# Optimization experiments

Hardware: AMD Instinct MI355X
Metric: run time of the kernel (lower is better)

## Reference

```python
import jax, jax.numpy as jnp
import numpy as np

B, N = 128, 128                      # graphs, nodes per graph (complete graphs)
D_IN, H, D_MP = 6, 32, 64            # GCN dims
SLOPE = 0.1                          # leaky_relu negative slope
E_UD = N * (N - 1) // 2              # undirected edges per graph
SMAT_IDX = np.array([0, 1, 2, 3, 1, 4, 5, 6, 2, 5, 7, 8, 3, 6, 8, 9])  # 10-vec -> sym 4x4


def setup_inputs():
    key = jax.random.key(0)
    ks = jax.random.split(key, 20)
    total = B * N
    # complete-graph connectivity (same topology for every graph, offset per graph)
    iu0, iu1 = np.triu_indices(N, 1)
    s = np.concatenate([iu0, iu1])
    d = np.concatenate([iu1, iu0])
    off = (np.arange(B) * N)[:, None]
    edge_index = np.stack([(off + s[None, :]).ravel(), (off + d[None, :]).ravel()])
    em = np.zeros((N, N), np.int32)
    em[iu0, iu1] = np.arange(E_UD)
    em[iu1, iu0] = np.arange(E_UD)
    ud_edges = np.stack([iu0, iu1], axis=1)

    def p(k, shape):
        return jax.random.normal(k, shape, jnp.float32) * 0.1

    return {
        "x": jax.random.normal(ks[0], (total, D_IN), jnp.float32),
        "edge_index": jnp.asarray(edge_index, jnp.int32),
        "edge_map": jnp.asarray(em, jnp.int32),
        "ud_edges": jnp.asarray(ud_edges, jnp.int32),
        # GCN stack 6->32->32->64
        "Wg0": p(ks[1], (D_IN, H)), "bg0": jnp.zeros((H,), jnp.float32),
        "Wg1": p(ks[2], (H, H)),    "bg1": jnp.zeros((H,), jnp.float32),
        "Wg2": p(ks[3], (H, D_MP)), "bg2": jnp.zeros((D_MP,), jnp.float32),
        # node MLP 64->64->64->10
        "Wn0": p(ks[4], (D_MP, D_MP)), "bn0": jnp.zeros((D_MP,), jnp.float32),
        "Wn1": p(ks[5], (D_MP, D_MP)), "bn1": jnp.zeros((D_MP,), jnp.float32),
        "Wn2": p(ks[6], (D_MP, 10)),   "bn2": jnp.zeros((10,), jnp.float32),
        # edge MLP 128->128->128->16
        "We0": p(ks[7], (2 * D_MP, 2 * D_MP)), "be0": jnp.zeros((2 * D_MP,), jnp.float32),
        "We1": p(ks[8], (2 * D_MP, 2 * D_MP)), "be1": jnp.zeros((2 * D_MP,), jnp.float32),
        "We2": p(ks[9], (2 * D_MP, 16)),       "be2": jnp.zeros((16,), jnp.float32),
    }


def _lrelu(h):
    return jnp.where(h >= 0, h, SLOPE * h)


def reference(x, edge_index, edge_map, ud_edges,
              Wg0, bg0, Wg1, bg1, Wg2, bg2,
              Wn0, bn0, Wn1, bn1, Wn2, bn2,
              We0, be0, We1, be1, We2, be2):
    total = x.shape[0]
    src, dst = edge_index[0], edge_index[1]
    x = x[:, :D_IN]  # node_feature_mode == 1

    # symmetric GCN normalization (no self loops): norm_e = deg_src^-1/2 * deg_dst^-1/2
    deg = jax.ops.segment_sum(jnp.ones(src.shape[0], x.dtype), dst, num_segments=total)
    dinv = jax.lax.rsqrt(jnp.maximum(deg, 1e-12))
    norm = (dinv[src] * dinv[dst])[:, None]

    def gcn(h, W, b):
        m = (h @ W)[src] * norm
        return jax.ops.segment_sum(m, dst, num_segments=total) + b

    h = _lrelu(gcn(x, Wg0, bg0))   # dropout skipped (eval mode)
    h = _lrelu(gcn(h, Wg1, bg1))
    h = gcn(h, Wg2, bg2)           # [total, 64]

    xb = h.reshape(B, N, D_MP)

    # batched node MLP (original loops per node)
    v = _lrelu(xb @ Wn0 + bn0)
    v = _lrelu(v @ Wn1 + bn1)
    v = v @ Wn2 + bn2              # [B, N, 10]

    # batched edge MLP for (i,j) ordering (original loops per edge; e_tril is
    # computed but discarded upstream since recover_factor is called with e_triu twice)
    xi = xb[:, ud_edges[:, 0]]
    xj = xb[:, ud_edges[:, 1]]
    e = jnp.concatenate([xi, xj], axis=-1)   # [B, E_UD, 128]
    e = _lrelu(e @ We0 + be0)
    e = _lrelu(e @ We1 + be1)
    e = e @ We2 + be2                        # [B, E_UD, 16]

    # assemble U: off-diagonal 4x4 blocks from e (both triangles), diagonal smat(v)
    blocks = e[:, edge_map]                  # [B, N, N, 16]
    diag = v[:, :, SMAT_IDX]                 # [B, N, 16]
    idx = jnp.arange(N)
    blocks = blocks.at[:, idx, idx].set(diag)
    U = blocks.reshape(B, N, N, 4, 4).transpose(0, 1, 3, 2, 4).reshape(B, 4 * N, 4 * N)
    return (h, U)
```

## Files before the change

### kernel.cpp

```cpp
#include <hip/hip_runtime.h>
#include <hip/hip_bf16.h>

#define LRELU(v) ((v) >= 0.f ? (v) : 0.1f*(v))

typedef float  f32x4 __attribute__((ext_vector_type(4)));
typedef short  s16x8 __attribute__((ext_vector_type(8)));
typedef int    i32x4 __attribute__((ext_vector_type(4)));
typedef unsigned short ushort_t;
typedef unsigned int   u32;

constexpr float GNORM = 1.0f/127.0f;

#define MFMA(d, a, b) d = __builtin_amdgcn_mfma_f32_16x16x32_bf16(a, b, d, 0, 0, 0)

__device__ __forceinline__ ushort_t f2bf(float v) {
    return __builtin_bit_cast(ushort_t, __float2bfloat16(v));
}
__device__ __forceinline__ float bf2f(ushort_t u) {
    return __builtin_bit_cast(float, (u32)u << 16);
}

__global__ __launch_bounds__(128) void k_gcn(
    const float* __restrict__ x,
    const float* __restrict__ Wg0, const float* __restrict__ bg0,
    const float* __restrict__ Wg1, const float* __restrict__ bg1,
    const float* __restrict__ Wg2, const float* __restrict__ bg2,
    float* __restrict__ hout)
{
    __shared__ __align__(16) float w0[192], w1[1024], w2[2048];
    __shared__ float bb0[32], bb1[32], bb2[64];
    __shared__ float ta[128][65];
    __shared__ float part[4][64];
    __shared__ float S[64];
    const int v = threadIdx.x;
    const int b = blockIdx.x;

    for (int idx = v; idx < 192;  idx += 128) w0[idx] = Wg0[idx];
    for (int idx = v; idx < 1024; idx += 128) w1[idx] = Wg1[idx];
    for (int idx = v; idx < 2048; idx += 128) w2[idx] = Wg2[idx];
    if (v < 32) { bb0[v] = bg0[v]; bb1[v] = bg1[v]; }
    if (v < 64) bb2[v] = bg2[v];

    float xv[6];
    #pragma unroll
    for (int k = 0; k < 6; ++k) xv[k] = x[(b*128 + v)*6 + k];
    __syncthreads();

    float t0[32];
    #pragma unroll
    for (int n = 0; n < 32; ++n) {
        float a = 0.f;
        #pragma unroll
        for (int k = 0; k < 6; ++k) a += xv[k]*w0[k*32+n];
        t0[n] = a;
        ta[v][n] = a;
    }
    __syncthreads();
    { const int g = v >> 5, d = v & 31;
      float p = 0.f;
      for (int r = 0; r < 32; ++r) p += ta[g*32+r][d];
      part[g][d] = p; }
    __syncthreads();
    if (v < 32) S[v] = part[0][v]+part[1][v]+part[2][v]+part[3][v];
    __syncthreads();
    float h1[32];
    #pragma unroll
    for (int n = 0; n < 32; ++n) {
        float hv = (S[n] - t0[n])*GNORM + bb0[n];
        h1[n] = LRELU(hv);
    }
    __syncthreads();

    float t1[32];
    #pragma unroll
    for (int n = 0; n < 32; ++n) t1[n] = 0.f;
    for (int k = 0; k < 32; ++k) {
        const float hk = h1[k];
        #pragma unroll
        for (int n4 = 0; n4 < 8; ++n4) {
            const float4 w = *(const float4*)&w1[k*32 + n4*4];
            t1[n4*4+0] += hk*w.x; t1[n4*4+1] += hk*w.y;
            t1[n4*4+2] += hk*w.z; t1[n4*4+3] += hk*w.w;
        }
    }
    #pragma unroll
    for (int n = 0; n < 32; ++n) ta[v][n] = t1[n];
    __syncthreads();
    { const int g = v >> 5, d = v & 31;
      float p = 0.f;
      for (int r = 0; r < 32; ++r) p += ta[g*32+r][d];
      part[g][d] = p; }
    __syncthreads();
    if (v < 32) S[v] = part[0][v]+part[1][v]+part[2][v]+part[3][v];
    __syncthreads();
    float h2[32];
    #pragma unroll
    for (int n = 0; n < 32; ++n) {
        float hv = (S[n] - t1[n])*GNORM + bb1[n];
        h2[n] = LRELU(hv);
    }
    __syncthreads();

    float t2[64];
    #pragma unroll
    for (int n = 0; n < 64; ++n) t2[n] = 0.f;
    for (int k = 0; k < 32; ++k) {
        const float hk = h2[k];
        #pragma unroll
        for (int n4 = 0; n4 < 16; ++n4) {
            const float4 w = *(const float4*)&w2[k*64 + n4*4];
            t2[n4*4+0] += hk*w.x; t2[n4*4+1] += hk*w.y;
            t2[n4*4+2] += hk*w.z; t2[n4*4+3] += hk*w.w;
        }
    }
    #pragma unroll
    for (int n = 0; n < 64; ++n) ta[v][n] = t2[n];
    __syncthreads();
    { const int g = v >> 5, d = v & 31;
      float p0 = 0.f, p1 = 0.f;
      for (int r = 0; r < 32; ++r) { p0 += ta[g*32+r][d]; p1 += ta[g*32+r][d+32]; }
      part[g][d] = p0; part[g][d+32] = p1; }
    __syncthreads();
    if (v < 64) S[v] = part[0][v]+part[1][v]+part[2][v]+part[3][v];
    __syncthreads();
    float* hrow = hout + (size_t)(b*128 + v)*64;
    #pragma unroll
    for (int n4 = 0; n4 < 16; ++n4) {
        float4 o;
        o.x = (S[n4*4+0] - t2[n4*4+0])*GNORM + bb2[n4*4+0];
        o.y = (S[n4*4+1] - t2[n4*4+1])*GNORM + bb2[n4*4+1];
        o.z = (S[n4*4+2] - t2[n4*4+2])*GNORM + bb2[n4*4+2];
        o.w = (S[n4*4+3] - t2[n4*4+3])*GNORM + bb2[n4*4+3];
        *(float4*)(hrow + n4*4) = o;
    }
}

__global__ __launch_bounds__(256) void k_nodemlp(
    const float* __restrict__ xb,
    const float* __restrict__ Wn0, const float* __restrict__ bn0,
    const float* __restrict__ Wn1, const float* __restrict__ bn1,
    const float* __restrict__ Wn2, const float* __restrict__ bn2,
    float* __restrict__ U)
{
    __shared__ __align__(16) float w0[4096], w1[4096], w2[640];
    __shared__ float bb0[64], bb1[64];
    __shared__ float bb2[16];
    __shared__ float xin[4][64], t1[4][64], t2[4][64], vb[4][10];
    const int tid = threadIdx.x;
    const int wv = tid >> 6, lane = tid & 63;
    const int node = blockIdx.x*4 + wv;

    for (int idx = tid; idx < 1024; idx += 256) {
        ((float4*)w0)[idx] = ((const float4*)Wn0)[idx];
        ((float4*)w1)[idx] = ((const float4*)Wn1)[idx];
    }
    for (int idx = tid; idx < 160; idx += 256)
        ((float4*)w2)[idx] = ((const float4*)Wn2)[idx];
    if (tid < 64) bb0[tid] = bn0[tid];
    else if (tid < 128) bb1[tid-64] = bn1[tid-64];
    else if (tid < 138) bb2[tid-128] = bn2[tid-128];
    xin[wv][lane] = xb[(size_t)node*64 + lane];
    __syncthreads();

    float a = bb0[lane];
    for (int k = 0; k < 64; ++k) a += xin[wv][k]*w0[k*64 + lane];
    t1[wv][lane] = LRELU(a);
    __syncthreads();

    float c = bb1[lane];
    for (int k = 0; k < 64; ++k) c += t1[wv][k]*w1[k*64 + lane];
    t2[wv][lane] = LRELU(c);
    __syncthreads();

    if (lane < 10) {
        float o = bb2[lane];
        for (int k = 0; k < 64; ++k) o += t2[wv][k]*w2[k*10 + lane];
        vb[wv][lane] = o;
    }
    __syncthreads();

    if (lane < 16) {
        const int m = (int)((0x9863875265413210ull >> (4*lane)) & 15ull);
        const int b = node >> 7, i = node & 127;
        U[(size_t)b*262144 + (size_t)(4*i + (lane>>2))*512 + 4*i + (lane&3)] = vb[wv][m];
    }
}

__global__ __launch_bounds__(128) void k_ab(
    const float* __restrict__ xb,
    const float* __restrict__ We0,
    float* __restrict__ Aout, float* __restrict__ Bout)
{
    __shared__ float xs[16][64];
    const int tid  = threadIdx.x;
    const int base = blockIdx.x * 16;
    for (int idx = tid; idx < 1024; idx += 128)
        xs[idx>>6][idx&63] = xb[(size_t)base*64 + idx];
    __syncthreads();

    float accA[16], accB[16];
    #pragma unroll
    for (int nd = 0; nd < 16; ++nd) { accA[nd] = 0.f; accB[nd] = 0.f; }
    for (int k = 0; k < 64; ++k) {
        const float wa = We0[k*128 + tid];
        const float wb = We0[(64+k)*128 + tid];
        #pragma unroll
        for (int nd = 0; nd < 16; ++nd) {
            const float xval = xs[nd][k];
            accA[nd] += xval*wa;
            accB[nd] += xval*wb;
        }
    }
    #pragma unroll
    for (int nd = 0; nd < 16; ++nd) {
        Aout[(size_t)(base+nd)*128 + tid] = accA[nd];
        Bout[(size_t)(base+nd)*128 + tid] = accB[nd];
    }
}

__global__ __launch_bounds__(256) void k_prep(
    const float* __restrict__ We1, const float* __restrict__ We2,
    ushort_t* __restrict__ BH, ushort_t* __restrict__ BM,
    ushort_t* __restrict__ W2H, ushort_t* __restrict__ W2M)
{
    const int gid = blockIdx.x*256 + threadIdx.x;
    if (gid < 16384) {
        const int k = gid >> 7, col = gid & 127;
        const float v = We1[gid];
        const ushort_t h = f2bf(v);
        const ushort_t m = f2bf(v - bf2f(h));
        const int cf = col >> 4, kc = (k >> 5) & 3;
        const int ln = ((k >> 3) & 3)*16 + (col & 15);
        const int e  = k & 7;
        const int off = ((cf*4 + kc)*64 + ln)*8 + e;
        BH[off] = h; BM[off] = m;
    }
    const int g2 = gid - 16384;
    if (g2 >= 0 && g2 < 2048) {
        const int k = g2 >> 4, n = g2 & 15;
        const float v = We2[g2];
        const ushort_t h = f2bf(v);
        const ushort_t m = f2bf(v - bf2f(h));
        const int kc = k >> 5;
        const int ln = ((k >> 3) & 3)*16 + n;
        const int e  = k & 7;
        const int off = (kc*64 + ln)*8 + e;
        W2H[off] = h; W2M[off] = m;
    }
}

__global__ __launch_bounds__(256, 4) void k_edge(
    const float* __restrict__ A, const float* __restrict__ Bt,
    const int* __restrict__ ud,
    const float* __restrict__ be0v,
    const ushort_t* __restrict__ BH, const ushort_t* __restrict__ BM,
    const float* __restrict__ be1v,
    const ushort_t* __restrict__ W2H, const ushort_t* __restrict__ W2M,
    const float* __restrict__ be2v,
    float* __restrict__ U)
{
    __shared__ __align__(16) char smem[32768];
    const int tid = threadIdx.x;
    const int wv = tid >> 6, lane = tid & 63;
    const int b = blockIdx.x / 127;
    const int t = blockIdx.x - b*127;
    const int* ud2 = ud + t*128;

    {
        const int s = lane;
        const int i  = ud2[2*s], jn = ud2[2*s+1];
        const int c0 = wv*32;
        const float* Ar = A  + (size_t)(b*128 + i )*128 + c0;
        const float* Br = Bt + (size_t)(b*128 + jn)*128 + c0;
        const int sw = (s & 7) << 4;
        char* rowh = smem + s*256;
        #pragma unroll
        for (int q = 0; q < 4; ++q) {
            const float4 a0 = ((const float4*)Ar)[2*q];
            const float4 a1 = ((const float4*)Ar)[2*q+1];
            const float4 b0 = ((const float4*)Br)[2*q];
            const float4 b1 = ((const float4*)Br)[2*q+1];
            const float4 e0 = ((const float4*)be0v)[wv*8 + 2*q];
            const float4 e1 = ((const float4*)be0v)[wv*8 + 2*q + 1];
            float vs[8] = {a0.x+b0.x+e0.x, a0.y+b0.y+e0.y, a0.z+b0.z+e0.z, a0.w+b0.w+e0.w,
                           a1.x+b1.x+e1.x, a1.y+b1.y+e1.y, a1.z+b1.z+e1.z, a1.w+b1.w+e1.w};
            ushort_t hb[8], mb[8];
            #pragma unroll
            for (int e = 0; e < 8; ++e) {
                const float v = LRELU(vs[e]);
                const ushort_t h = f2bf(v);
                hb[e] = h;
                mb[e] = f2bf(v - bf2f(h));
            }
            const int off = (64*wv + 16*q) ^ sw;
            *(s16x8*)(rowh + off)         = *(const s16x8*)hb;
            *(s16x8*)(rowh + 16384 + off) = *(const s16x8*)mb;
        }
    }
    __syncthreads();

    f32x4 acc[4][2];
    #pragma unroll
    for (int rf = 0; rf < 4; ++rf) {
        acc[rf][0] = (f32x4){0.f,0.f,0.f,0.f};
        acc[rf][1] = (f32x4){0.f,0.f,0.f,0.f};
    }
    {
        const int arow = lane & 15;
        const int klo  = (lane >> 4) * 16;
        #pragma unroll
        for (int kc = 0; kc < 4; ++kc) {
            s16x8 bh[2], bm[2];
            #pragma unroll
            for (int c = 0; c < 2; ++c) {
                const int boff = (((wv*2 + c)*4 + kc)*64 + lane)*8;
                bh[c] = *(const s16x8*)(BH + boff);
                bm[c] = *(const s16x8*)(BM + boff);
            }
            const int kb = kc*64 + klo;
            #pragma unroll
            for (int rf = 0; rf < 4; ++rf) {
                const int row = rf*16 + arow;
                const int off = row*256 + (kb ^ ((row & 7) << 4));
                const s16x8 ah = *(const s16x8*)(smem + off);
                const s16x8 am = *(const s16x8*)(smem + 16384 + off);
                MFMA(acc[rf][0], ah, bh[0]);
                MFMA(acc[rf][0], ah, bm[0]);
                MFMA(acc[rf][0], am, bh[0]);
                MFMA(acc[rf][1], ah, bh[1]);
                MFMA(acc[rf][1], ah, bm[1]);
                MFMA(acc[rf][1], am, bh[1]);
            }
        }
    }
    __syncthreads();

    {
        const int ccol = lane & 15;
        const int crow = (lane >> 4) * 4;
        #pragma unroll
        for (int c = 0; c < 2; ++c) {
            const int col = wv*32 + c*16 + ccol;
            const float b1 = be1v[col];
            const int col4 = col*4;
            #pragma unroll
            for (int rf = 0; rf < 4; ++rf) {
                #pragma unroll
                for (int r = 0; r < 4; ++r) {
                    const int row = rf*16 + crow + r;
                    const float v = LRELU(acc[rf][c][r] + b1);
                    const ushort_t h = f2bf(v);
                    const ushort_t m = f2bf(v - bf2f(h));
                    const u32 word = ((u32)m << 16) | (u32)h;
                    *(u32*)(smem + row*512 + (col4 ^ ((row & 7) << 4))) = word;
                }
            }
        }
    }
    __syncthreads();

    {
        const int row = wv*16 + (lane & 15);
        const int sw  = (row & 7) << 4;
        const char* rb = smem + row*512;
        f32x4 acc2 = (f32x4){0.f,0.f,0.f,0.f};
        #pragma unroll
        for (int kc = 0; kc < 4; ++kc) {
            const int kb = kc*128 + (lane >> 4)*32;
            const i32x4 w0 = *(const i32x4*)(rb + (kb ^ sw));
            const i32x4 w1 = *(const i32x4*)(rb + ((kb + 16) ^ sw));
            i32x4 hv, mv;
            hv[0] = (int)__builtin_amdgcn_perm((u32)w0[1], (u32)w0[0], 0x05040100u);
            hv[1] = (int)__builtin_amdgcn_perm((u32)w0[3], (u32)w0[2], 0x05040100u);
            hv[2] = (int)__builtin_amdgcn_perm((u32)w1[1], (u32)w1[0], 0x05040100u);
            hv[3] = (int)__builtin_amdgcn_perm((u32)w1[3], (u32)w1[2], 0x05040100u);
            mv[0] = (int)__builtin_amdgcn_perm((u32)w0[1], (u32)w0[0], 0x07060302u);
            mv[1] = (int)__builtin_amdgcn_perm((u32)w0[3], (u32)w0[2], 0x07060302u);
            mv[2] = (int)__builtin_amdgcn_perm((u32)w1[1], (u32)w1[0], 0x07060302u);
            mv[3] = (int)__builtin_amdgcn_perm((u32)w1[3], (u32)w1[2], 0x07060302u);
            const s16x8 ah = __builtin_bit_cast(s16x8, hv);
            const s16x8 am = __builtin_bit_cast(s16x8, mv);
            const int woff = (kc*64 + lane)*8;
            const s16x8 wh = *(const s16x8*)(W2H + woff);
            const s16x8 wm = *(const s16x8*)(W2M + woff);
            MFMA(acc2, ah, wh);
            MFMA(acc2, ah, wm);
            MFMA(acc2, am, wh);
        }
        const int col = lane & 15;
        const float b2 = be2v[col];
        const int p = col >> 2, q = col & 3;
        float* Ub = U + (size_t)b*262144;
        #pragma unroll
        for (int r = 0; r < 4; ++r) {
            const int s = wv*16 + (lane >> 4)*4 + r;
            const int i  = ud2[2*s], jn = ud2[2*s+1];
            const float v = acc2[r] + b2;
            Ub[(size_t)(4*i  + p)*512 + 4*jn + q] = v;
            Ub[(size_t)(4*jn + p)*512 + 4*i  + q] = v;
        }
    }
}

extern "C" void kernel_launch(void* const* d_in, const int* in_sizes, int n_in,
                              void* d_out, int out_size, void* d_ws, size_t ws_size,
                              hipStream_t stream)
{
    const float* x   = (const float*)d_in[0];
    const int*   ud  = (const int*)  d_in[3];
    const float* Wg0 = (const float*)d_in[4];
    const float* bg0 = (const float*)d_in[5];
    const float* Wg1 = (const float*)d_in[6];
    const float* bg1 = (const float*)d_in[7];
    const float* Wg2 = (const float*)d_in[8];
    const float* bg2 = (const float*)d_in[9];
    const float* Wn0 = (const float*)d_in[10];
    const float* bn0 = (const float*)d_in[11];
    const float* Wn1 = (const float*)d_in[12];
    const float* bn1 = (const float*)d_in[13];
    const float* Wn2 = (const float*)d_in[14];
    const float* bn2 = (const float*)d_in[15];
    const float* We0 = (const float*)d_in[16];
    const float* be0 = (const float*)d_in[17];
    const float* We1 = (const float*)d_in[18];
    const float* be1 = (const float*)d_in[19];
    const float* We2 = (const float*)d_in[20];
    const float* be2 = (const float*)d_in[21];

    float* hout = (float*)d_out;
    float* U    = (float*)d_out + 1048576;
    float* Aw   = (float*)d_ws;
    float* Bw   = Aw + (size_t)16384*128;
    ushort_t* BH  = (ushort_t*)((char*)d_ws + (size_t)2*16384*128*4);
    ushort_t* BM  = BH + 16384;
    ushort_t* W2H = BM + 16384;
    ushort_t* W2M = W2H + 2048;

    k_gcn<<<dim3(128), dim3(128), 0, stream>>>(x, Wg0,bg0, Wg1,bg1, Wg2,bg2, hout);
    k_prep<<<dim3(72), dim3(256), 0, stream>>>(We1, We2, BH, BM, W2H, W2M);
    k_ab<<<dim3(1024), dim3(128), 0, stream>>>(hout, We0, Aw, Bw);
    k_edge<<<dim3(128*127), dim3(256), 0, stream>>>(Aw, Bw, ud, be0,
                                                    BH, BM, be1, W2H, W2M, be2, U);
    k_nodemlp<<<dim3(4096), dim3(256), 0, stream>>>(hout, Wn0,bn0, Wn1,bn1, Wn2,bn2, U);
}
```

Measured before the change: 419.1 us.

## Restructure edge kernel to two tiles per block with prefetch and vector stores

The edge kernel now processes two edge tiles per workgroup. It prefetches the next tile's A/B rows into registers during the epilogue, hoists biases and W2 fragments, and remaps block IDs across batches. Output is staged through shared memory so each 4x4 block row is written with float4 stores instead of scalar scatters. The be0 bias moves into k_ab, and k_gcn and k_ab are widened to 256 threads by splitting output columns or nodes across two halves. The cost is more register pressure from the prefetch buffers, extra barriers, and a serialized tail tile in the last workgroup of each batch.

```diff
diff --git a/kernel.cpp b/kernel.cpp
--- a/kernel.cpp
+++ b/kernel.cpp
@@ -20,7 +20,7 @@
     return __builtin_bit_cast(float, (u32)u << 16);
 }
 
-__global__ __launch_bounds__(128) void k_gcn(
+__global__ __launch_bounds__(256) void k_gcn(
     const float* __restrict__ x,
     const float* __restrict__ Wg0, const float* __restrict__ bg0,
     const float* __restrict__ Wg1, const float* __restrict__ bg1,
@@ -29,108 +29,115 @@
 {
     __shared__ __align__(16) float w0[192], w1[1024], w2[2048];
     __shared__ float bb0[32], bb1[32], bb2[64];
-    __shared__ float ta[128][65];
-    __shared__ float part[4][64];
+    __shared__ float ta[128][33];
+    __shared__ float tc[128][65];
+    __shared__ float part[8][64];
     __shared__ float S[64];
-    const int v = threadIdx.x;
+    const int tid = threadIdx.x;
+    const int v = tid & 127, hf = tid >> 7;
     const int b = blockIdx.x;
 
-    for (int idx = v; idx < 192;  idx += 128) w0[idx] = Wg0[idx];
-    for (int idx = v; idx < 1024; idx += 128) w1[idx] = Wg1[idx];
-    for (int idx = v; idx < 2048; idx += 128) w2[idx] = Wg2[idx];
-    if (v < 32) { bb0[v] = bg0[v]; bb1[v] = bg1[v]; }
-    if (v < 64) bb2[v] = bg2[v];
+    for (int idx = tid; idx < 192;  idx += 256) w0[idx] = Wg0[idx];
+    for (int idx = tid; idx < 1024; idx += 256) w1[idx] = Wg1[idx];
+    for (int idx = tid; idx < 2048; idx += 256) w2[idx] = Wg2[idx];
+    if (tid < 32) { bb0[tid] = bg0[tid]; bb1[tid] = bg1[tid]; }
+    if (tid >= 64 && tid < 128) bb2[tid-64] = bg2[tid-64];
 
     float xv[6];
     #pragma unroll
     for (int k = 0; k < 6; ++k) xv[k] = x[(b*128 + v)*6 + k];
     __syncthreads();
 
-    float t0[32];
-    #pragma unroll
-    for (int n = 0; n < 32; ++n) {
+    const int rg = tid >> 5, rd = tid & 31;
+    const int rg2 = tid >> 6, rd2 = tid & 63;
+
+    float t0[16];
+    #pragma unroll
+    for (int n = 0; n < 16; ++n) {
         float a = 0.f;
         #pragma unroll
-        for (int k = 0; k < 6; ++k) a += xv[k]*w0[k*32+n];
-        t0[n] = a;
-        ta[v][n] = a;
-    }
-    __syncthreads();
-    { const int g = v >> 5, d = v & 31;
-      float p = 0.f;
-      for (int r = 0; r < 32; ++r) p += ta[g*32+r][d];
-      part[g][d] = p; }
-    __syncthreads();
-    if (v < 32) S[v] = part[0][v]+part[1][v]+part[2][v]+part[3][v];
-    __syncthreads();
-    float h1[32];
-    #pragma unroll
-    for (int n = 0; n < 32; ++n) {
-        float hv = (S[n] - t0[n])*GNORM + bb0[n];
+        for (int k = 0; k < 6; ++k) a += xv[k]*w0[k*32 + hf*16 + n];
+        t0[n] = a; ta[v][hf*16+n] = a;
+    }
+    __syncthreads();
+    { float p = 0.f;
+      for (int r = 0; r < 16; ++r) p += ta[rg*16+r][rd];
+      part[rg][rd] = p; }
+    __syncthreads();
+    if (tid < 32) S[tid] = part[0][tid]+part[1][tid]+part[2][tid]+part[3][tid]
+                          +part[4][tid]+part[5][tid]+part[6][tid]+part[7][tid];
+    __syncthreads();
+    float h1[16];
+    #pragma unroll
+    for (int n = 0; n < 16; ++n) {
+        float hv = (S[hf*16+n] - t0[n])*GNORM + bb0[hf*16+n];
         h1[n] = LRELU(hv);
-    }
-    __syncthreads();
-
-    float t1[32];
-    #pragma unroll
-    for (int n = 0; n < 32; ++n) t1[n] = 0.f;
+        ta[v][hf*16+n] = h1[n];
+    }
+    __syncthreads();
+
+    float t1[16];
+    #pragma unroll
+    for (int n = 0; n < 16; ++n) t1[n] = 0.f;
     for (int k = 0; k < 32; ++k) {
-        const float hk = h1[k];
-        #pragma unroll
-        for (int n4 = 0; n4 < 8; ++n4) {
-            const float4 w = *(const float4*)&w1[k*32 + n4*4];
+        const float hk = ta[v][k];
+        #pragma unroll
+        for (int n4 = 0; n4 < 4; ++n4) {
+            const float4 w = *(const float4*)&w1[k*32 + hf*16 + n4*4];
             t1[n4*4+0] += hk*w.x; t1[n4*4+1] += hk*w.y;
             t1[n4*4+2] += hk*w.z; t1[n4*4+3] += hk*w.w;
         }
     }
-    #pragma unroll
-    for (int n = 0; n < 32; ++n) ta[v][n] = t1[n];
-    __syncthreads();
-    { const int g = v >> 5, d = v & 31;
-      float p = 0.f;
-      for (int r = 0; r < 32; ++r) p += ta[g*32+r][d];
-      part[g][d] = p; }
-    __syncthreads();
-    if (v < 32) S[v] = part[0][v]+part[1][v]+part[2][v]+part[3][v];
-    __syncthreads();
-    float h2[32];
-    #pragma unroll
-    for (int n = 0; n < 32; ++n) {
-        float hv = (S[n] - t1[n])*GNORM + bb1[n];
+    __syncthreads();
+    #pragma unroll
+    for (int n = 0; n < 16; ++n) ta[v][hf*16+n] = t1[n];
+    __syncthreads();
+    { float p = 0.f;
+      for (int r = 0; r < 16; ++r) p += ta[rg*16+r][rd];
+      part[rg][rd] = p; }
+    __syncthreads();
+    if (tid < 32) S[tid] = part[0][tid]+part[1][tid]+part[2][tid]+part[3][tid]
+                          +part[4][tid]+part[5][tid]+part[6][tid]+part[7][tid];
+    __syncthreads();
+    float h2[16];
+    #pragma unroll
+    for (int n = 0; n < 16; ++n) {
+        float hv = (S[hf*16+n] - t1[n])*GNORM + bb1[hf*16+n];
         h2[n] = LRELU(hv);
-    }
-    __syncthreads();
-
-    float t2[64];
-    #pragma unroll
-    for (int n = 0; n < 64; ++n) t2[n] = 0.f;
+        ta[v][hf*16+n] = h2[n];
+    }
+    __syncthreads();
+
+    float t2[32];
+    #pragma unroll
+    for (int n = 0; n < 32; ++n) t2[n] = 0.f;
     for (int k = 0; k < 32; ++k) {
-        const float hk = h2[k];
-        #pragma unroll
-        for (int n4 = 0; n4 < 16; ++n4) {
-            const float4 w = *(const float4*)&w2[k*64 + n4*4];
+        const float hk = ta[v][k];
+        #pragma unroll
+        for (int n4 = 0; n4 < 8; ++n4) {
+            const float4 w = *(const float4*)&w2[k*64 + hf*32 + n4*4];
             t2[n4*4+0] += hk*w.x; t2[n4*4+1] += hk*w.y;
             t2[n4*4+2] += hk*w.z; t2[n4*4+3] += hk*w.w;
         }
     }
-    #pragma unroll
-    for (int n = 0; n < 64; ++n) ta[v][n] = t2[n];
-    __syncthreads();
-    { const int g = v >> 5, d = v & 31;
-      float p0 = 0.f, p1 = 0.f;
-      for (int r = 0; r < 32; ++r) { p0 += ta[g*32+r][d]; p1 += ta[g*32+r][d+32]; }
-      part[g][d] = p0; part[g][d+32] = p1; }
-    __syncthreads();
-    if (v < 64) S[v] = part[0][v]+part[1][v]+part[2][v]+part[3][v];
-    __syncthreads();
-    float* hrow = hout + (size_t)(b*128 + v)*64;
-    #pragma unroll
-    for (int n4 = 0; n4 < 16; ++n4) {
+    __syncthreads();
+    #pragma unroll
+    for (int n = 0; n < 32; ++n) tc[v][hf*32+n] = t2[n];
+    __syncthreads();
+    { float p = 0.f;
+      for (int r = 0; r < 32; ++r) p += tc[rg2*32+r][rd2];
+      part[rg2][rd2] = p; }
+    __syncthreads();
+    if (tid < 64) S[tid] = part[0][tid]+part[1][tid]+part[2][tid]+part[3][tid];
+    __syncthreads();
+    float* hrow = hout + (size_t)(b*128 + v)*64 + hf*32;
+    #pragma unroll
+    for (int n4 = 0; n4 < 8; ++n4) {
         float4 o;
-        o.x = (S[n4*4+0] - t2[n4*4+0])*GNORM + bb2[n4*4+0];
-        o.y = (S[n4*4+1] - t2[n4*4+1])*GNORM + bb2[n4*4+1];
-        o.z = (S[n4*4+2] - t2[n4*4+2])*GNORM + bb2[n4*4+2];
-        o.w = (S[n4*4+3] - t2[n4*4+3])*GNORM + bb2[n4*4+3];
+        o.x = (S[hf*32+n4*4+0] - t2[n4*4+0])*GNORM + bb2[hf*32+n4*4+0];
+        o.y = (S[hf*32+n4*4+1] - t2[n4*4+1])*GNORM + bb2[hf*32+n4*4+1];
+        o.z = (S[hf*32+n4*4+2] - t2[n4*4+2])*GNORM + bb2[hf*32+n4*4+2];
+        o.w = (S[hf*32+n4*4+3] - t2[n4*4+3])*GNORM + bb2[hf*32+n4*4+3];
         *(float4*)(hrow + n4*4) = o;
     }
 }
@@ -186,35 +193,37 @@
     }
 }
 
-__global__ __launch_bounds__(128) void k_ab(
+__global__ __launch_bounds__(256) void k_ab(
     const float* __restrict__ xb,
-    const float* __restrict__ We0,
+    const float* __restrict__ We0, const float* __restrict__ be0v,
     float* __restrict__ Aout, float* __restrict__ Bout)
 {
     __shared__ float xs[16][64];
     const int tid  = threadIdx.x;
+    const int col  = tid & 127, nh = tid >> 7;
     const int base = blockIdx.x * 16;
-    for (int idx = tid; idx < 1024; idx += 128)
+    for (int idx = tid; idx < 1024; idx += 256)
         xs[idx>>6][idx&63] = xb[(size_t)base*64 + idx];
     __syncthreads();
 
-    float accA[16], accB[16];
-    #pragma unroll
-    for (int nd = 0; nd < 16; ++nd) { accA[nd] = 0.f; accB[nd] = 0.f; }
+    float accA[8], accB[8];
+    #pragma unroll
+    for (int nd = 0; nd < 8; ++nd) { accA[nd] = 0.f; accB[nd] = 0.f; }
     for (int k = 0; k < 64; ++k) {
-        const float wa = We0[k*128 + tid];
-        const float wb = We0[(64+k)*128 + tid];
-        #pragma unroll
-        for (int nd = 0; nd < 16; ++nd) {
-            const float xval = xs[nd][k];
+        const float wa = We0[k*128 + col];
+        const float wb = We0[(64+k)*128 + col];
+        #pragma unroll
+        for (int nd = 0; nd < 8; ++nd) {
+            const float xval = xs[nh*8+nd][k];
             accA[nd] += xval*wa;
             accB[nd] += xval*wb;
         }
     }
-    #pragma unroll
-    for (int nd = 0; nd < 16; ++nd) {
-        Aout[(size_t)(base+nd)*128 + tid] = accA[nd];
-        Bout[(size_t)(base+nd)*128 + tid] = accB[nd];
+    const float bias = be0v[col];
+    #pragma unroll
+    for (int nd = 0; nd < 8; ++nd) {
+        Aout[(size_t)(base+nh*8+nd)*128 + col] = accA[nd] + bias;
+        Bout[(size_t)(base+nh*8+nd)*128 + col] = accB[nd];
     }
 }
 
@@ -252,7 +261,6 @@
 __global__ __launch_bounds__(256, 4) void k_edge(
     const float* __restrict__ A, const float* __restrict__ Bt,
     const int* __restrict__ ud,
-    const float* __restrict__ be0v,
     const ushort_t* __restrict__ BH, const ushort_t* __restrict__ BM,
     const float* __restrict__ be1v,
     const ushort_t* __restrict__ W2H, const ushort_t* __restrict__ W2M,
@@ -262,143 +270,171 @@
     __shared__ __align__(16) char smem[32768];
     const int tid = threadIdx.x;
     const int wv = tid >> 6, lane = tid & 63;
-    const int b = blockIdx.x / 127;
-    const int t = blockIdx.x - b*127;
-    const int* ud2 = ud + t*128;
-
+    const int wg = (blockIdx.x & 7)*1024 + (blockIdx.x >> 3);
+    const int b  = wg >> 6;
+    const int w0 = wg & 63;
+    const int t0 = 2*w0;
+    const int nt = (w0 == 63) ? 1 : 2;
+
+    const float be2  = be2v[lane & 15];
+    const float be1c0 = be1v[wv*32 + (lane & 15)];
+    const float be1c1 = be1v[wv*32 + 16 + (lane & 15)];
+    const float* Ab = A  + (size_t)b*16384;
+    const float* Bb = Bt + (size_t)b*16384;
+    float* Ub = U + (size_t)b*262144;
+
+    float4 pa[8], pb[8];
     {
-        const int s = lane;
-        const int i  = ud2[2*s], jn = ud2[2*s+1];
-        const int c0 = wv*32;
-        const float* Ar = A  + (size_t)(b*128 + i )*128 + c0;
-        const float* Br = Bt + (size_t)(b*128 + jn)*128 + c0;
-        const int sw = (s & 7) << 4;
-        char* rowh = smem + s*256;
-        #pragma unroll
-        for (int q = 0; q < 4; ++q) {
-            const float4 a0 = ((const float4*)Ar)[2*q];
-            const float4 a1 = ((const float4*)Ar)[2*q+1];
-            const float4 b0 = ((const float4*)Br)[2*q];
-            const float4 b1 = ((const float4*)Br)[2*q+1];
-            const float4 e0 = ((const float4*)be0v)[wv*8 + 2*q];
-            const float4 e1 = ((const float4*)be0v)[wv*8 + 2*q + 1];
-            float vs[8] = {a0.x+b0.x+e0.x, a0.y+b0.y+e0.y, a0.z+b0.z+e0.z, a0.w+b0.w+e0.w,
-                           a1.x+b1.x+e1.x, a1.y+b1.y+e1.y, a1.z+b1.z+e1.z, a1.w+b1.w+e1.w};
-            ushort_t hb[8], mb[8];
-            #pragma unroll
-            for (int e = 0; e < 8; ++e) {
-                const float v = LRELU(vs[e]);
-                const ushort_t h = f2bf(v);
-                hb[e] = h;
-                mb[e] = f2bf(v - bf2f(h));
+        const int2 ij1 = *(const int2*)(ud + t0*128 + 2*lane);
+        const float4* Ar = (const float4*)(Ab + (size_t)ij1.x*128 + wv*32);
+        const float4* Br = (const float4*)(Bb + (size_t)ij1.y*128 + wv*32);
+        #pragma unroll
+        for (int q = 0; q < 8; ++q) { pa[q] = Ar[q]; pb[q] = Br[q]; }
+    }
+
+    for (int ti = 0; ti < nt; ++ti) {
+        const int t = t0 + ti;
+
+        {
+            const int sw = (lane & 7) << 4;
+            char* rowh = smem + lane*256;
+            #pragma unroll
+            for (int q = 0; q < 4; ++q) {
+                const float4 a0 = pa[2*q], a1 = pa[2*q+1];
+                const float4 b0 = pb[2*q], b1 = pb[2*q+1];
+                float vs[8] = {a0.x+b0.x, a0.y+b0.y, a0.z+b0.z, a0.w+b0.w,
+                               a1.x+b1.x, a1.y+b1.y, a1.z+b1.z, a1.w+b1.w};
+                ushort_t hb[8], mb[8];
+                #pragma unroll
+                for (int e = 0; e < 8; ++e) {
+                    const float vv = LRELU(vs[e]);
+                    const ushort_t h = f2bf(vv);
+                    hb[e] = h;
+                    mb[e] = f2bf(vv - bf2f(h));
+                }
+                const int off = (64*wv + 16*q) ^ sw;
+                *(s16x8*)(rowh + off)         = *(const s16x8*)hb;
+                *(s16x8*)(rowh + 16384 + off) = *(const s16x8*)mb;
             }
-            const int off = (64*wv + 16*q) ^ sw;
-            *(s16x8*)(rowh + off)         = *(const s16x8*)hb;
-            *(s16x8*)(rowh + 16384 + off) = *(const s16x8*)mb;
-        }
-    }
-    __syncthreads();
-
-    f32x4 acc[4][2];
-    #pragma unroll
-    for (int rf = 0; rf < 4; ++rf) {
-        acc[rf][0] = (f32x4){0.f,0.f,0.f,0.f};
-        acc[rf][1] = (f32x4){0.f,0.f,0.f,0.f};
-    }
-    {
-        const int arow = lane & 15;
-        const int klo  = (lane >> 4) * 16;
-        #pragma unroll
-        for (int kc = 0; kc < 4; ++kc) {
-            s16x8 bh[2], bm[2];
-            #pragma unroll
-            for (int c = 0; c < 2; ++c) {
-                const int boff = (((wv*2 + c)*4 + kc)*64 + lane)*8;
-                bh[c] = *(const s16x8*)(BH + boff);
-                bm[c] = *(const s16x8*)(BM + boff);
-            }
-            const int kb = kc*64 + klo;
-            #pragma unroll
-            for (int rf = 0; rf < 4; ++rf) {
-                const int row = rf*16 + arow;
-                const int off = row*256 + (kb ^ ((row & 7) << 4));
-                const s16x8 ah = *(const s16x8*)(smem + off);
-                const s16x8 am = *(const s16x8*)(smem + 16384 + off);
-                MFMA(acc[rf][0], ah, bh[0]);
-                MFMA(acc[rf][0], ah, bm[0]);
-                MFMA(acc[rf][0], am, bh[0]);
-                MFMA(acc[rf][1], ah, bh[1]);
-                MFMA(acc[rf][1], ah, bm[1]);
-                MFMA(acc[rf][1], am, bh[1]);
-            }
-        }
-    }
-    __syncthreads();
-
-    {
-        const int ccol = lane & 15;
-        const int crow = (lane >> 4) * 4;
-        #pragma unroll
-        for (int c = 0; c < 2; ++c) {
-            const int col = wv*32 + c*16 + ccol;
-            const float b1 = be1v[col];
-            const int col4 = col*4;
-            #pragma unroll
-            for (int rf = 0; rf < 4; ++rf) {
+        }
+        __syncthreads();
+
+        f32x4 acc[4][2];
+        #pragma unroll
+        for (int rf = 0; rf < 4; ++rf) {
+            acc[rf][0] = (f32x4){0.f,0.f,0.f,0.f};
+            acc[rf][1] = (f32x4){0.f,0.f,0.f,0.f};
+        }
+        {
+            const int arow = lane & 15;
+            const int klo  = (lane >> 4) * 16;
+            #pragma unroll
+            for (int kc = 0; kc < 4; ++kc) {
+                const int o0 = (((wv*2 + 0)*4 + kc)*64 + lane)*8;
+                const int o1 = (((wv*2 + 1)*4 + kc)*64 + lane)*8;
+                const s16x8 bh0 = *(const s16x8*)(BH + o0);
+                const s16x8 bm0 = *(const s16x8*)(BM + o0);
+                const s16x8 bh1 = *(const s16x8*)(BH + o1);
+                const s16x8 bm1 = *(const s16x8*)(BM + o1);
+                const int kb = kc*64 + klo;
                 #pragma unroll
-                for (int r = 0; r < 4; ++r) {
-                    const int row = rf*16 + crow + r;
-                    const float v = LRELU(acc[rf][c][r] + b1);
-                    const ushort_t h = f2bf(v);
-                    const ushort_t m = f2bf(v - bf2f(h));
-                    const u32 word = ((u32)m << 16) | (u32)h;
-                    *(u32*)(smem + row*512 + (col4 ^ ((row & 7) << 4))) = word;
+                for (int rf = 0; rf < 4; ++rf) {
+                    const int row = rf*16 + arow;
+                    const int off = row*256 + (kb ^ ((row & 7) << 4));
+                    const s16x8 ah = *(const s16x8*)(smem + off);
+                    const s16x8 am = *(const s16x8*)(smem + 16384 + off);
+                    MFMA(acc[rf][0], ah, bh0);
+                    MFMA(acc[rf][0], ah, bm0);
+                    MFMA(acc[rf][0], am, bh0);
+                    MFMA(acc[rf][1], ah, bh1);
+                    MFMA(acc[rf][1], ah, bm1);
+                    MFMA(acc[rf][1], am, bh1);
                 }
             }
         }
-    }
-    __syncthreads();
-
-    {
-        const int row = wv*16 + (lane & 15);
-        const int sw  = (row & 7) << 4;
-        const char* rb = smem + row*512;
-        f32x4 acc2 = (f32x4){0.f,0.f,0.f,0.f};
+        __syncthreads();
+
+        int2 ijn;
+        const bool more = (ti + 1 < nt);
+        if (more) ijn = *(const int2*)(ud + (t+1)*128 + 2*lane);
+
+        {
+            const int ccol = lane & 15;
+            const int crow = (lane >> 4) * 4;
+            #pragma unroll
+            for (int c = 0; c < 2; ++c) {
+                const float b1 = c ? be1c1 : be1c0;
+                const int col4 = (wv*32 + c*16 + ccol)*4;
+                #pragma unroll
+                for (int rf = 0; rf < 4; ++rf) {
+                    #pragma unroll
+                    for (int r = 0; r < 4; ++r) {
+                        const int row = rf*16 + crow + r;
+                        const float v = LRELU(acc[rf][c][r] + b1);
+                        const ushort_t h = f2bf(v);
+                        const ushort_t m = f2bf(v - bf2f(h));
+                        const u32 word = ((u32)m << 16) | (u32)h;
+                        *(u32*)(smem + row*512 + (col4 ^ ((row & 7) << 4))) = word;
+                    }
+                }
+            }
+        }
+
+        if (more) {
+            const float4* Arn = (const float4*)(Ab + (size_t)ijn.x*128 + wv*32);
+            const float4* Brn = (const float4*)(Bb + (size_t)ijn.y*128 + wv*32);
+            #pragma unroll
+            for (int q = 0; q < 8; ++q) { pa[q] = Arn[q]; pb[q] = Brn[q]; }
+        }
+        s16x8 w2h[4], w2m[4];
         #pragma unroll
         for (int kc = 0; kc < 4; ++kc) {
-            const int kb = kc*128 + (lane >> 4)*32;
-            const i32x4 w0 = *(const i32x4*)(rb + (kb ^ sw));
-            const i32x4 w1 = *(const i32x4*)(rb + ((kb + 16) ^ sw));
-            i32x4 hv, mv;
-            hv[0] = (int)__builtin_amdgcn_perm((u32)w0[1], (u32)w0[0], 0x05040100u);
-            hv[1] = (int)__builtin_amdgcn_perm((u32)w0[3], (u32)w0[2], 0x05040100u);
-            hv[2] = (int)__builtin_amdgcn_perm((u32)w1[1], (u32)w1[0], 0x05040100u);
-            hv[3] = (int)__builtin_amdgcn_perm((u32)w1[3], (u32)w1[2], 0x05040100u);
-            mv[0] = (int)__builtin_amdgcn_perm((u32)w0[1], (u32)w0[0], 0x07060302u);
-            mv[1] = (int)__builtin_amdgcn_perm((u32)w0[3], (u32)w0[2], 0x07060302u);
-            mv[2] = (int)__builtin_amdgcn_perm((u32)w1[1], (u32)w1[0], 0x07060302u);
-            mv[3] = (int)__builtin_amdgcn_perm((u32)w1[3], (u32)w1[2], 0x07060302u);
-            const s16x8 ah = __builtin_bit_cast(s16x8, hv);
-            const s16x8 am = __builtin_bit_cast(s16x8, mv);
             const int woff = (kc*64 + lane)*8;
-            const s16x8 wh = *(const s16x8*)(W2H + woff);
-            const s16x8 wm = *(const s16x8*)(W2M + woff);
-            MFMA(acc2, ah, wh);
-            MFMA(acc2, ah, wm);
-            MFMA(acc2, am, wh);
-        }
-        const int col = lane & 15;
-        const float b2 = be2v[col];
-        const int p = col >> 2, q = col & 3;
-        float* Ub = U + (size_t)b*262144;
-        #pragma unroll
-        for (int r = 0; r < 4; ++r) {
-            const int s = wv*16 + (lane >> 4)*4 + r;
-            const int i  = ud2[2*s], jn = ud2[2*s+1];
-            const float v = acc2[r] + b2;
-            Ub[(size_t)(4*i  + p)*512 + 4*jn + q] = v;
-            Ub[(size_t)(4*jn + p)*512 + 4*i  + q] = v;
-        }
+            w2h[kc] = *(const s16x8*)(W2H + woff);
+            w2m[kc] = *(const s16x8*)(W2M + woff);
+        }
+        __syncthreads();
+
+        {
+            const int row = wv*16 + (lane & 15);
+            const int swr = (row & 7) << 4;
+            const char* rb = smem + row*512;
+            f32x4 acc2 = (f32x4){0.f,0.f,0.f,0.f};
+            #pragma unroll
+            for (int kc = 0; kc < 4; ++kc) {
+                const int kb = kc*128 + (lane >> 4)*32;
+                const i32x4 wd0 = *(const i32x4*)(rb + (kb ^ swr));
+                const i32x4 wd1 = *(const i32x4*)(rb + ((kb + 16) ^ swr));
+                i32x4 hv, mv;
+                hv[0] = (int)__builtin_amdgcn_perm((u32)wd0[1], (u32)wd0[0], 0x05040100u);
+                hv[1] = (int)__builtin_amdgcn_perm((u32)wd0[3], (u32)wd0[2], 0x05040100u);
+                hv[2] = (int)__builtin_amdgcn_perm((u32)wd1[1], (u32)wd1[0], 0x05040100u);
+                hv[3] = (int)__builtin_amdgcn_perm((u32)wd1[3], (u32)wd1[2], 0x05040100u);
+                mv[0] = (int)__builtin_amdgcn_perm((u32)wd0[1], (u32)wd0[0], 0x07060302u);
+                mv[1] = (int)__builtin_amdgcn_perm((u32)wd0[3], (u32)wd0[2], 0x07060302u);
+                mv[2] = (int)__builtin_amdgcn_perm((u32)wd1[1], (u32)wd1[0], 0x07060302u);
+                mv[3] = (int)__builtin_amdgcn_perm((u32)wd1[3], (u32)wd1[2], 0x07060302u);
+                const s16x8 ah = __builtin_bit_cast(s16x8, hv);
+                const s16x8 am = __builtin_bit_cast(s16x8, mv);
+                MFMA(acc2, ah, w2h[kc]);
+                MFMA(acc2, ah, w2m[kc]);
+                MFMA(acc2, am, w2h[kc]);
+            }
+
+            const int sloc = lane >> 2;
+            const int p    = lane & 3;
+            const int2 ij3 = *(const int2*)(ud + t*128 + 2*(wv*16 + sloc));
+            char* scr = smem + wv*8192;
+            const int c16 = lane & 15, hi = lane >> 4;
+            #pragma unroll
+            for (int r = 0; r < 4; ++r)
+                *(float*)(scr + (hi*4 + r)*80 + c16*4) = acc2[r] + be2;
+            const f32x4 rv = *(const f32x4*)(scr + sloc*80 + p*16);
+            float4 o; o.x = rv[0]; o.y = rv[1]; o.z = rv[2]; o.w = rv[3];
+            *(float4*)(Ub + (size_t)(4*ij3.x + p)*512 + 4*ij3.y) = o;
+            *(float4*)(Ub + (size_t)(4*ij3.y + p)*512 + 4*ij3.x) = o;
+        }
+        __syncthreads();
     }
 }
 
@@ -436,10 +472,10 @@
     ushort_t* W2H = BM + 16384;
     ushort_t* W2M = W2H + 2048;
 
-    k_gcn<<<dim3(128), dim3(128), 0, stream>>>(x, Wg0,bg0, Wg1,bg1, Wg2,bg2, hout);
     k_prep<<<dim3(72), dim3(256), 0, stream>>>(We1, We2, BH, BM, W2H, W2M);
-    k_ab<<<dim3(1024), dim3(128), 0, stream>>>(hout, We0, Aw, Bw);
-    k_edge<<<dim3(128*127), dim3(256), 0, stream>>>(Aw, Bw, ud, be0,
-                                                    BH, BM, be1, W2H, W2M, be2, U);
+    k_gcn<<<dim3(128), dim3(256), 0, stream>>>(x, Wg0,bg0, Wg1,bg1, Wg2,bg2, hout);
+    k_ab<<<dim3(1024), dim3(256), 0, stream>>>(hout, We0, be0, Aw, Bw);
+    k_edge<<<dim3(8192), dim3(256), 0, stream>>>(Aw, Bw, ud,
+                                                 BH, BM, be1, W2H, W2M, be2, U);
     k_nodemlp<<<dim3(4096), dim3(256), 0, stream>>>(hout, Wn0,bn0, Wn1,bn1, Wn2,bn2, U);
 }
```

Measured after the change: 964.5 us. 130% more time.
